# Performance work log

Hardware: AMD Instinct MI355X
Metric: run time of the kernel (lower is better)

## Reference

```python
import jax, jax.numpy as jnp
import numpy as np

A, B, M, H, MAX_NB, N_MOLS = 100000, 200000, 20000, 256, 10, 2000
ATOM_FDIM, BOND_FDIM, DEPTH = 35, 5, 3


def setup_inputs() -> dict:
    key = jax.random.key(0)
    ks = jax.random.split(key, 10)
    fatoms = jax.random.normal(ks[0], (A, ATOM_FDIM), dtype=jnp.float32)
    fbonds = jax.random.normal(ks[1], (B, ATOM_FDIM + BOND_FDIM), dtype=jnp.float32)
    agraph = jax.random.randint(ks[2], (A, MAX_NB), 0, M + B)
    bgraph = jax.random.randint(ks[3], (B, MAX_NB), 0, M + B)
    tree_message = jax.random.normal(ks[4], (M, H), dtype=jnp.float32)
    tree_message = tree_message.at[0].set(0.0)  # all_mess[0] is the zero pad vector
    atom_scope = jnp.sort(jax.random.randint(ks[5], (A,), 0, N_MOLS))
    s = 1.0 / np.sqrt(H)
    W_i = jax.random.normal(ks[6], (ATOM_FDIM + BOND_FDIM, H), dtype=jnp.float32) * s
    W_h = jax.random.normal(ks[7], (H, H), dtype=jnp.float32) * s
    W_o_w = jax.random.normal(ks[8], (ATOM_FDIM + H, H), dtype=jnp.float32) * s
    W_o_b = jax.random.normal(ks[9], (H,), dtype=jnp.float32) * s
    return {"fatoms": fatoms, "fbonds": fbonds, "agraph": agraph, "bgraph": bgraph,
            "tree_message": tree_message, "atom_scope": atom_scope,
            "W_i": W_i, "W_h": W_h, "W_o_w": W_o_w, "W_o_b": W_o_b}


def reference(fatoms, fbonds, agraph, bgraph, tree_message, atom_scope, W_i, W_h, W_o_w, W_o_b):
    binput = fbonds @ W_i                       # [B, H]
    graph_message = jax.nn.relu(binput)
    for _ in range(DEPTH - 1):
        message = jnp.concatenate([tree_message, graph_message], axis=0)  # [M+B, H]
        nei = message[bgraph].sum(axis=1)       # gather [B, MAX_NB, H] -> sum -> [B, H]
        graph_message = jax.nn.relu(binput + nei @ W_h)
    message = jnp.concatenate([tree_message, graph_message], axis=0)
    nei = message[agraph].sum(axis=1)           # [A, H]
    ainput = jnp.concatenate([fatoms, nei], axis=1)  # [A, ATOM_FDIM + H]
    atom_hiddens = jax.nn.relu(ainput @ W_o_w + W_o_b)
    # scope-based segment-mean pooling over atoms of each molecule
    sums = jax.ops.segment_sum(atom_hiddens, atom_scope, num_segments=N_MOLS)
    counts = jax.ops.segment_sum(jnp.ones((atom_hiddens.shape[0],), atom_hiddens.dtype),
                                 atom_scope, num_segments=N_MOLS)
    return sums / jnp.maximum(counts, 1.0)[:, None]
```

## Files before the change

kernel.cpp:

```cpp
#include <hip/hip_runtime.h>
#include <cstdint>
#include <cstddef>

#define A_N 100000
#define B_N 200000
#define M_N 20000
#define POOL_N 220000
#define HD 256
#define MAX_NB 10
#define N_MOLS 2000
#define ATOM_FDIM 35
#define FB_DIM 40

typedef unsigned short u16;
typedef __attribute__((ext_vector_type(8))) short bf16x8;
typedef __attribute__((ext_vector_type(4))) float f32x4;

__device__ u16 g_msg0[(size_t)B_N * HD];
__device__ u16 g_msg1[(size_t)B_N * HD];
__device__ u16 g_tmsgh[(size_t)M_N * HD];
__device__ u16 g_P[(size_t)POOL_N * HD];
__device__ u16 g_Q[(size_t)POOL_N * HD];
__device__ u16 g_binH[(size_t)B_N * HD];
__device__ u16 g_Fh[(size_t)A_N * HD];
__device__ u16 g_pWh_hi[65536], g_pWh_lo[65536];
__device__ u16 g_pWo_hi[65536], g_pWo_lo[65536];
__device__ int g_mstart[N_MOLS + 1];

__device__ __forceinline__ u16 f2b(float f)
{
    union { float f; unsigned u; } x; x.f = f;
    const unsigned r = x.u + 0x7FFFu + ((x.u >> 16) & 1u);
    return (u16)(r >> 16);
}
__device__ __forceinline__ float b2f(u16 h) { return __uint_as_float((unsigned)h << 16); }
__device__ __forceinline__ float blo(unsigned u) { return __uint_as_float(u << 16); }
__device__ __forceinline__ float bhi(unsigned u) { return __uint_as_float(u & 0xffff0000u); }

__device__ __forceinline__ int lbound(const int* __restrict__ s, int n, int v)
{
    int l = 0, r = n;
    while (l < r) { const int mid = (l + r) >> 1; if (s[mid] < v) l = mid + 1; else r = mid; }
    return l;
}

__device__ __forceinline__ void gl_lds16(const u16* g, u16* l)
{
    __builtin_amdgcn_global_load_lds(
        (const __attribute__((address_space(1))) unsigned int*)g,
        (__attribute__((address_space(3))) unsigned int*)l,
        16, 0, 0);
}

__global__ __launch_bounds__(256)
void k_setup(const float* __restrict__ tmsg,
             const float* __restrict__ Wh, const float* __restrict__ Wo,
             const int* __restrict__ scope)
{
    const int bid = blockIdx.x;
    const int tid = threadIdx.x;
    if (bid < 5000) {
        const int i = (bid * 256 + tid) * 4;
        if (i < M_N * HD) {
            const float4 v = *(const float4*)(tmsg + i);
            ushort4 o;
            o.x = f2b(v.x); o.y = f2b(v.y); o.z = f2b(v.z); o.w = f2b(v.w);
            *(ushort4*)(g_tmsgh + i) = o;
        }
    } else if (bid < 5032) {
        const int id = (bid - 5000) * 256 + tid;
        const int l = id & 63;
        const int t = (id >> 6) & 15;
        const int c = id >> 10;
        const int n = t * 16 + (l & 15);
        const int kb = c * 32 + ((l >> 4) << 3);
        const size_t base = (size_t)id * 8;
        #pragma unroll
        for (int j = 0; j < 8; ++j) {
            const int k = kb + j;
            const float wh = Wh[(size_t)k * HD + n];
            const u16 hh = f2b(wh);
            g_pWh_hi[base + j] = hh;
            g_pWh_lo[base + j] = f2b(wh - b2f(hh));
            const float wo = Wo[(size_t)(35 + k) * HD + n];
            const u16 oh = f2b(wo);
            g_pWo_hi[base + j] = oh;
            g_pWo_lo[base + j] = f2b(wo - b2f(oh));
        }
    } else {
        const int m = (bid - 5032) * 256 + tid;
        if (m <= N_MOLS) g_mstart[m] = lbound(scope, A_N, m);
    }
}

__global__ __launch_bounds__(256, 4)
void k_in(const float* __restrict__ fbonds, const float* __restrict__ Wi)
{
    const int lane = threadIdx.x & 63;
    const int wv   = threadIdx.x >> 6;
    const int c    = (wv & 1) * 128 + lane * 2;
    const int pair = (blockIdx.x * 4 + wv) >> 1;
    const int np   = gridDim.x * 2;

    float2 w[FB_DIM];
    #pragma unroll
    for (int k = 0; k < FB_DIM; ++k)
        w[k] = *(const float2*)&Wi[(size_t)k * HD + c];

    #pragma unroll 1
    for (int row = pair; row < B_N; row += np) {
        const float* fr = fbonds + (size_t)row * FB_DIM;
        float ax = 0.f, ay = 0.f;
        #pragma unroll
        for (int q = 0; q < FB_DIM / 4; ++q) {
            const float4 fv = *(const float4*)(fr + q * 4);
            ax += fv.x * w[q*4+0].x; ay += fv.x * w[q*4+0].y;
            ax += fv.y * w[q*4+1].x; ay += fv.y * w[q*4+1].y;
            ax += fv.z * w[q*4+2].x; ay += fv.z * w[q*4+2].y;
            ax += fv.w * w[q*4+3].x; ay += fv.w * w[q*4+3].y;
        }
        const size_t base = (size_t)row * HD + c;
        ushort2 bi; bi.x = f2b(ax); bi.y = f2b(ay);
        *(ushort2*)(g_binH + base) = bi;
        ushort2 o; o.x = f2b(fmaxf(ax, 0.f)); o.y = f2b(fmaxf(ay, 0.f));
        *(ushort2*)(g_msg0 + base) = o;
    }
}

__global__ __launch_bounds__(256, 2)
void k_gemmMF(int sel, int rowStart, int rowEnd)
{
    const u16* msrc = (sel == 1) ? g_msg1 : g_msg0;
    const u16* pHi  = (sel == 2) ? g_pWo_hi : g_pWh_hi;
    const u16* pLo  = (sel == 2) ? g_pWo_lo : g_pWh_lo;
    u16* dst        = (sel == 2) ? g_Q : g_P;

    __shared__ u16 lds[2][16384];

    const int tid  = threadIdx.x;
    const int lane = tid & 63;
    const int wv   = tid >> 6;
    const int l15  = lane & 15;
    const int quad = lane >> 4;
    const int tOff = (wv & 1) * 8;

    int rowIdeal[4];
    const u16* srow[4];
    #pragma unroll
    for (int rg = 0; rg < 4; ++rg) {
        const int ri = rowStart + blockIdx.x * 128 + (wv >> 1) * 64 + rg * 16 + l15;
        rowIdeal[rg] = ri;
        const int r = (ri < rowEnd) ? ri : (rowEnd - 1);
        srow[rg] = (r < M_N) ? (g_tmsgh + (size_t)r * HD)
                             : (msrc + (size_t)(r - M_N) * HD);
    }

    #define STAGE(bf, cc) do {                                            \
        const u16* sh_ = pHi + (cc) * 8192 + tid * 8;                     \
        const u16* sl_ = pLo + (cc) * 8192 + tid * 8;                     \
        u16* dh_ = &lds[bf][tid * 8];                                     \
        u16* dl_ = &lds[bf][8192 + tid * 8];                              \
        gl_lds16(sh_,        dh_);                                        \
        gl_lds16(sh_ + 2048, dh_ + 2048);                                 \
        gl_lds16(sh_ + 4096, dh_ + 4096);                                 \
        gl_lds16(sh_ + 6144, dh_ + 6144);                                 \
        gl_lds16(sl_,        dl_);                                        \
        gl_lds16(sl_ + 2048, dl_ + 2048);                                 \
        gl_lds16(sl_ + 4096, dl_ + 4096);                                 \
        gl_lds16(sl_ + 6144, dl_ + 6144);                                 \
    } while (0)

    f32x4 acc[4][8];
    #pragma unroll
    for (int rg = 0; rg < 4; ++rg)
        #pragma unroll
        for (int t = 0; t < 8; ++t)
            acc[rg][t] = (f32x4){0.f, 0.f, 0.f, 0.f};

    STAGE(0, 0);
    bf16x8 b0 = *(const bf16x8*)(srow[0] + quad * 8);
    bf16x8 b1 = *(const bf16x8*)(srow[1] + quad * 8);
    bf16x8 b2 = *(const bf16x8*)(srow[2] + quad * 8);
    bf16x8 b3 = *(const bf16x8*)(srow[3] + quad * 8);

    #pragma unroll 1
    for (int c = 0; c < 8; ++c) {
        __syncthreads();
        if (c < 7) STAGE((c + 1) & 1, c + 1);

        const int cn = (c + 1) & 7;
        const bf16x8 n0 = *(const bf16x8*)(srow[0] + cn * 32 + quad * 8);
        const bf16x8 n1 = *(const bf16x8*)(srow[1] + cn * 32 + quad * 8);
        const bf16x8 n2 = *(const bf16x8*)(srow[2] + cn * 32 + quad * 8);
        const bf16x8 n3 = *(const bf16x8*)(srow[3] + cn * 32 + quad * 8);

        const u16* Lh = &lds[c & 1][(size_t)tOff * 512 + lane * 8];
        const u16* Ll = Lh + 8192;
        #pragma unroll
        for (int t = 0; t < 8; ++t) {
            const bf16x8 ah = *(const bf16x8*)(Lh + t * 512);
            acc[0][t] = __builtin_amdgcn_mfma_f32_16x16x32_bf16(ah, b0, acc[0][t], 0, 0, 0);
            acc[1][t] = __builtin_amdgcn_mfma_f32_16x16x32_bf16(ah, b1, acc[1][t], 0, 0, 0);
            acc[2][t] = __builtin_amdgcn_mfma_f32_16x16x32_bf16(ah, b2, acc[2][t], 0, 0, 0);
            acc[3][t] = __builtin_amdgcn_mfma_f32_16x16x32_bf16(ah, b3, acc[3][t], 0, 0, 0);
            const bf16x8 al = *(const bf16x8*)(Ll + t * 512);
            acc[0][t] = __builtin_amdgcn_mfma_f32_16x16x32_bf16(al, b0, acc[0][t], 0, 0, 0);
            acc[1][t] = __builtin_amdgcn_mfma_f32_16x16x32_bf16(al, b1, acc[1][t], 0, 0, 0);
            acc[2][t] = __builtin_amdgcn_mfma_f32_16x16x32_bf16(al, b2, acc[2][t], 0, 0, 0);
            acc[3][t] = __builtin_amdgcn_mfma_f32_16x16x32_bf16(al, b3, acc[3][t], 0, 0, 0);
        }
        b0 = n0; b1 = n1; b2 = n2; b3 = n3;
    }
    #undef STAGE

    #pragma unroll
    for (int rg = 0; rg < 4; ++rg) {
        if (rowIdeal[rg] < rowEnd) {
            u16* drow = dst + (size_t)rowIdeal[rg] * HD + tOff * 16 + quad * 4;
            #pragma unroll
            for (int t = 0; t < 8; ++t) {
                ushort4 o;
                o.x = f2b(acc[rg][t][0]); o.y = f2b(acc[rg][t][1]);
                o.z = f2b(acc[rg][t][2]); o.w = f2b(acc[rg][t][3]);
                *(ushort4*)(drow + t * 16) = o;
            }
        }
    }
}

__global__ __launch_bounds__(256)
void k_gather(const int* __restrict__ bgraph, int dstSel, int rowOff)
{
    u16* dst = dstSel ? g_msg1 : g_msg0;
    __shared__ int idx_s[8][MAX_NB];
    const int tid = threadIdx.x;
    const int rowBase = rowOff + blockIdx.x * 8;
    if (tid < 8 * MAX_NB) {
        const int r = tid / MAX_NB;
        const int j = tid - r * MAX_NB;
        idx_s[r][j] = bgraph[(size_t)(rowBase + r) * MAX_NB + j];
    }
    __syncthreads();
    const int rl = tid >> 5;
    const int c  = (tid & 31) << 3;
    const int row = rowBase + rl;

    const uint4 bv = *(const uint4*)(g_binH + (size_t)row * HD + c);
    float s[8] = {0.f,0.f,0.f,0.f,0.f,0.f,0.f,0.f};
    #pragma unroll
    for (int j = 0; j < MAX_NB; ++j) {
        const uint4 v = *(const uint4*)(g_P + (size_t)idx_s[rl][j] * HD + c);
        s[0] += blo(v.x); s[1] += bhi(v.x);
        s[2] += blo(v.y); s[3] += bhi(v.y);
        s[4] += blo(v.z); s[5] += bhi(v.z);
        s[6] += blo(v.w); s[7] += bhi(v.w);
    }
    uint4 w;
    w.x = ((unsigned)f2b(fmaxf(s[0] + blo(bv.x), 0.f)))
        | ((unsigned)f2b(fmaxf(s[1] + bhi(bv.x), 0.f)) << 16);
    w.y = ((unsigned)f2b(fmaxf(s[2] + blo(bv.y), 0.f)))
        | ((unsigned)f2b(fmaxf(s[3] + bhi(bv.y), 0.f)) << 16);
    w.z = ((unsigned)f2b(fmaxf(s[4] + blo(bv.z), 0.f)))
        | ((unsigned)f2b(fmaxf(s[5] + bhi(bv.z), 0.f)) << 16);
    w.w = ((unsigned)f2b(fmaxf(s[6] + blo(bv.w), 0.f)))
        | ((unsigned)f2b(fmaxf(s[7] + bhi(bv.w), 0.f)) << 16);
    *(uint4*)(dst + (size_t)row * HD + c) = w;
}

__global__ __launch_bounds__(256, 4)
void k_F(const float* __restrict__ fatoms, const float* __restrict__ Wo,
         const float* __restrict__ bias)
{
    const int lane = threadIdx.x & 63;
    const int wv   = threadIdx.x >> 6;
    const int c    = (wv & 1) * 128 + lane * 2;
    const int pair = (blockIdx.x * 4 + wv) >> 1;
    const int np   = gridDim.x * 2;

    float2 w[ATOM_FDIM];
    #pragma unroll
    for (int k = 0; k < ATOM_FDIM; ++k)
        w[k] = *(const float2*)&Wo[(size_t)k * HD + c];
    const float2 b2 = *(const float2*)&bias[c];

    #pragma unroll 1
    for (int row = pair; row < A_N; row += np) {
        const float* fr = fatoms + (size_t)row * ATOM_FDIM;
        float ax = b2.x, ay = b2.y;
        #pragma unroll
        for (int q = 0; q < 8; ++q) {
            const float4 fv = *(const float4*)(fr + q * 4);
            ax += fv.x * w[q*4+0].x; ay += fv.x * w[q*4+0].y;
            ax += fv.y * w[q*4+1].x; ay += fv.y * w[q*4+1].y;
            ax += fv.z * w[q*4+2].x; ay += fv.z * w[q*4+2].y;
            ax += fv.w * w[q*4+3].x; ay += fv.w * w[q*4+3].y;
        }
        #pragma unroll
        for (int k = 32; k < ATOM_FDIM; ++k) {
            const float f = fr[k];
            ax += f * w[k].x; ay += f * w[k].y;
        }
        const size_t base = (size_t)row * HD + c;
        ushort2 o; o.x = f2b(ax); o.y = f2b(ay);
        *(ushort2*)(g_Fh + base) = o;
    }
}

__global__ __launch_bounds__(256)
void k_gatherA(const int* __restrict__ agraph, float* __restrict__ out)
{
    const int mol = blockIdx.x >> 1;
    const int ch  = (blockIdx.x & 1) * 128;
    const int tid = threadIdx.x;
    const int grp = tid >> 4;
    const int lc  = (tid & 15) * 8;
    const int c   = ch + lc;

    const int s0 = g_mstart[mol];
    const int s1 = g_mstart[mol + 1];

    float s[8] = {0.f,0.f,0.f,0.f,0.f,0.f,0.f,0.f};
    #pragma unroll 1
    for (int a = s0 + grp; a < s1; a += 16) {
        const int* ap = agraph + (size_t)a * MAX_NB;
        int idx[MAX_NB];
        #pragma unroll
        for (int j = 0; j < MAX_NB; ++j) idx[j] = ap[j];
        const uint4 fv = *(const uint4*)(g_Fh + (size_t)a * HD + c);
        float g0=0.f,g1=0.f,g2=0.f,g3=0.f,g4=0.f,g5=0.f,g6=0.f,g7=0.f;
        #pragma unroll
        for (int j = 0; j < MAX_NB; ++j) {
            const uint4 v = *(const uint4*)(g_Q + (size_t)idx[j] * HD + c);
            g0 += blo(v.x); g1 += bhi(v.x);
            g2 += blo(v.y); g3 += bhi(v.y);
            g4 += blo(v.z); g5 += bhi(v.z);
            g6 += blo(v.w); g7 += bhi(v.w);
        }
        s[0] += fmaxf(g0 + blo(fv.x), 0.f); s[1] += fmaxf(g1 + bhi(fv.x), 0.f);
        s[2] += fmaxf(g2 + blo(fv.y), 0.f); s[3] += fmaxf(g3 + bhi(fv.y), 0.f);
        s[4] += fmaxf(g4 + blo(fv.z), 0.f); s[5] += fmaxf(g5 + bhi(fv.z), 0.f);
        s[6] += fmaxf(g6 + blo(fv.w), 0.f); s[7] += fmaxf(g7 + bhi(fv.w), 0.f);
    }

    __shared__ float red[16][128];
    #pragma unroll
    for (int q = 0; q < 8; ++q) red[grp][lc + q] = s[q];
    __syncthreads();
    if (tid < 128) {
        float acc = 0.f;
        #pragma unroll
        for (int g = 0; g < 16; ++g) acc += red[g][tid];
        const float inv = 1.0f / fmaxf((float)(s1 - s0), 1.0f);
        out[(size_t)mol * HD + ch + tid] = acc * inv;
    }
}

extern "C" void kernel_launch(void* const* d_in, const int* in_sizes, int n_in,
                              void* d_out, int out_size, void* d_ws, size_t ws_size,
                              hipStream_t stream)
{
    const float* fatoms = (const float*)d_in[0];
    const float* fbonds = (const float*)d_in[1];
    const int*   agraph = (const int*)d_in[2];
    const int*   bgraph = (const int*)d_in[3];
    const float* tmsg   = (const float*)d_in[4];
    const int*   scope  = (const int*)d_in[5];
    const float* W_i    = (const float*)d_in[6];
    const float* W_h    = (const float*)d_in[7];
    const float* W_o    = (const float*)d_in[8];
    const float* W_ob   = (const float*)d_in[9];
    float* out = (float*)d_out;

    (void)d_ws; (void)ws_size;

    k_setup<<<5040, 256, 0, stream>>>(tmsg, W_h, W_o, scope);
    k_in<<<1024, 256, 0, stream>>>(fbonds, W_i);

    k_gemmMF<<<(POOL_N + 127) / 128, 256, 0, stream>>>(0, 0, POOL_N);
    for (int ch = 0; ch < 4; ++ch)
        k_gather<<<B_N / 32, 256, 0, stream>>>(bgraph, 1, ch * (B_N / 4));
    k_gemmMF<<<(B_N + 127) / 128, 256, 0, stream>>>(1, M_N, POOL_N);
    for (int ch = 0; ch < 4; ++ch)
        k_gather<<<B_N / 32, 256, 0, stream>>>(bgraph, 0, ch * (B_N / 4));

    k_gemmMF<<<(POOL_N + 127) / 128, 256, 0, stream>>>(2, 0, POOL_N);
    k_F<<<1024, 256, 0, stream>>>(fatoms, W_o, W_ob);
    k_gatherA<<<N_MOLS * 2, 256, 0, stream>>>(agraph, out);
}
```

Measured before the change: 1.209 ms.

## Stage feature rows in LDS for input projections and split gatherA over four chunks

k_in and k_F now copy 64-row tiles of fbonds/fatoms into shared memory with gl_lds16. Each thread then computes one output column across all tiled rows, instead of each wave re-reading rows from global memory with float2 weights. The aim is coalesced feature loads and less redundant global traffic, at the cost of narrower 2-byte stores and a serial 64-row inner loop. k_gatherA is split into four 64-column chunks per molecule with 32 row groups, which gives more blocks and more parallelism over atoms.

```diff
diff --git a/kernel.cpp b/kernel.cpp
--- a/kernel.cpp
+++ b/kernel.cpp
@@ -93,37 +93,42 @@
     }
 }
 
-__global__ __launch_bounds__(256, 4)
+__global__ __launch_bounds__(256)
 void k_in(const float* __restrict__ fbonds, const float* __restrict__ Wi)
 {
-    const int lane = threadIdx.x & 63;
-    const int wv   = threadIdx.x >> 6;
-    const int c    = (wv & 1) * 128 + lane * 2;
-    const int pair = (blockIdx.x * 4 + wv) >> 1;
-    const int np   = gridDim.x * 2;
-
-    float2 w[FB_DIM];
-    #pragma unroll
-    for (int k = 0; k < FB_DIM; ++k)
-        w[k] = *(const float2*)&Wi[(size_t)k * HD + c];
-
+    __shared__ float Lf[64 * FB_DIM];
+    const int tid = threadIdx.x;
+
+    float w[FB_DIM];
+    #pragma unroll
+    for (int k = 0; k < FB_DIM; ++k) w[k] = Wi[(size_t)k * HD + tid];
+
+    const int ntile = B_N / 64;
     #pragma unroll 1
-    for (int row = pair; row < B_N; row += np) {
-        const float* fr = fbonds + (size_t)row * FB_DIM;
-        float ax = 0.f, ay = 0.f;
-        #pragma unroll
-        for (int q = 0; q < FB_DIM / 4; ++q) {
-            const float4 fv = *(const float4*)(fr + q * 4);
-            ax += fv.x * w[q*4+0].x; ay += fv.x * w[q*4+0].y;
-            ax += fv.y * w[q*4+1].x; ay += fv.y * w[q*4+1].y;
-            ax += fv.z * w[q*4+2].x; ay += fv.z * w[q*4+2].y;
-            ax += fv.w * w[q*4+3].x; ay += fv.w * w[q*4+3].y;
-        }
-        const size_t base = (size_t)row * HD + c;
-        ushort2 bi; bi.x = f2b(ax); bi.y = f2b(ay);
-        *(ushort2*)(g_binH + base) = bi;
-        ushort2 o; o.x = f2b(fmaxf(ax, 0.f)); o.y = f2b(fmaxf(ay, 0.f));
-        *(ushort2*)(g_msg0 + base) = o;
+    for (int t = blockIdx.x; t < ntile; t += gridDim.x) {
+        const float* src = fbonds + (size_t)t * (64 * FB_DIM);
+        __syncthreads();
+        #pragma unroll
+        for (int i = 0; i < 3; ++i) {
+            const int g = i * 256 + tid;
+            if (g < 640) gl_lds16((const u16*)(src + g * 4), (u16*)(Lf + g * 4));
+        }
+        __syncthreads();
+        #pragma unroll 1
+        for (int r = 0; r < 64; ++r) {
+            const float* fr = Lf + r * FB_DIM;
+            float a0 = 0.f, a1 = 0.f;
+            #pragma unroll
+            for (int q = 0; q < FB_DIM / 4; ++q) {
+                const float4 fv = *(const float4*)(fr + q * 4);
+                a0 += fv.x * w[q*4+0] + fv.z * w[q*4+2];
+                a1 += fv.y * w[q*4+1] + fv.w * w[q*4+3];
+            }
+            const float acc = a0 + a1;
+            const size_t base = (size_t)(t * 64 + r) * HD + tid;
+            g_binH[base] = f2b(acc);
+            g_msg0[base] = f2b(fmaxf(acc, 0.f));
+        }
     }
 }
 
@@ -267,61 +272,64 @@
     *(uint4*)(dst + (size_t)row * HD + c) = w;
 }
 
-__global__ __launch_bounds__(256, 4)
+__global__ __launch_bounds__(256)
 void k_F(const float* __restrict__ fatoms, const float* __restrict__ Wo,
          const float* __restrict__ bias)
 {
-    const int lane = threadIdx.x & 63;
-    const int wv   = threadIdx.x >> 6;
-    const int c    = (wv & 1) * 128 + lane * 2;
-    const int pair = (blockIdx.x * 4 + wv) >> 1;
-    const int np   = gridDim.x * 2;
-
-    float2 w[ATOM_FDIM];
-    #pragma unroll
-    for (int k = 0; k < ATOM_FDIM; ++k)
-        w[k] = *(const float2*)&Wo[(size_t)k * HD + c];
-    const float2 b2 = *(const float2*)&bias[c];
-
+    __shared__ float Lf[64 * ATOM_FDIM];
+    const int tid = threadIdx.x;
+
+    float w[ATOM_FDIM];
+    #pragma unroll
+    for (int k = 0; k < ATOM_FDIM; ++k) w[k] = Wo[(size_t)k * HD + tid];
+    const float b = bias[tid];
+
+    const int ntile = (A_N + 63) / 64;
     #pragma unroll 1
-    for (int row = pair; row < A_N; row += np) {
-        const float* fr = fatoms + (size_t)row * ATOM_FDIM;
-        float ax = b2.x, ay = b2.y;
-        #pragma unroll
-        for (int q = 0; q < 8; ++q) {
-            const float4 fv = *(const float4*)(fr + q * 4);
-            ax += fv.x * w[q*4+0].x; ay += fv.x * w[q*4+0].y;
-            ax += fv.y * w[q*4+1].x; ay += fv.y * w[q*4+1].y;
-            ax += fv.z * w[q*4+2].x; ay += fv.z * w[q*4+2].y;
-            ax += fv.w * w[q*4+3].x; ay += fv.w * w[q*4+3].y;
-        }
-        #pragma unroll
-        for (int k = 32; k < ATOM_FDIM; ++k) {
-            const float f = fr[k];
-            ax += f * w[k].x; ay += f * w[k].y;
-        }
-        const size_t base = (size_t)row * HD + c;
-        ushort2 o; o.x = f2b(ax); o.y = f2b(ay);
-        *(ushort2*)(g_Fh + base) = o;
+    for (int t = blockIdx.x; t < ntile; t += gridDim.x) {
+        const int rows = (t * 64 + 64 <= A_N) ? 64 : (A_N - t * 64);
+        const int ng = rows * ATOM_FDIM / 4;
+        const float* src = fatoms + (size_t)t * (64 * ATOM_FDIM);
+        __syncthreads();
+        #pragma unroll
+        for (int i = 0; i < 3; ++i) {
+            const int g = i * 256 + tid;
+            if (g < ng) gl_lds16((const u16*)(src + g * 4), (u16*)(Lf + g * 4));
+        }
+        __syncthreads();
+        #pragma unroll 1
+        for (int r = 0; r < rows; ++r) {
+            const float* fr = Lf + r * ATOM_FDIM;
+            float a0 = b, a1 = 0.f;
+            #pragma unroll
+            for (int q = 0; q < 8; ++q) {
+                const float4 fv = *(const float4*)(fr + q * 4);
+                a0 += fv.x * w[q*4+0] + fv.z * w[q*4+2];
+                a1 += fv.y * w[q*4+1] + fv.w * w[q*4+3];
+            }
+            a0 += fr[32] * w[32] + fr[34] * w[34];
+            a1 += fr[33] * w[33];
+            g_Fh[(size_t)(t * 64 + r) * HD + tid] = f2b(a0 + a1);
+        }
     }
 }
 
 __global__ __launch_bounds__(256)
 void k_gatherA(const int* __restrict__ agraph, float* __restrict__ out)
 {
-    const int mol = blockIdx.x >> 1;
-    const int ch  = (blockIdx.x & 1) * 128;
-    const int tid = threadIdx.x;
-    const int grp = tid >> 4;
-    const int lc  = (tid & 15) * 8;
-    const int c   = ch + lc;
+    const int mol = blockIdx.x >> 2;
+    const int q   = blockIdx.x & 3;
+    const int tid = threadIdx.x;
+    const int grp = tid >> 3;
+    const int lc  = (tid & 7) * 8;
+    const int c   = q * 64 + lc;
 
     const int s0 = g_mstart[mol];
     const int s1 = g_mstart[mol + 1];
 
     float s[8] = {0.f,0.f,0.f,0.f,0.f,0.f,0.f,0.f};
     #pragma unroll 1
-    for (int a = s0 + grp; a < s1; a += 16) {
+    for (int a = s0 + grp; a < s1; a += 32) {
         const int* ap = agraph + (size_t)a * MAX_NB;
         int idx[MAX_NB];
         #pragma unroll
@@ -342,16 +350,16 @@
         s[6] += fmaxf(g6 + blo(fv.w), 0.f); s[7] += fmaxf(g7 + bhi(fv.w), 0.f);
     }
 
-    __shared__ float red[16][128];
-    #pragma unroll
-    for (int q = 0; q < 8; ++q) red[grp][lc + q] = s[q];
+    __shared__ float red[32][64];
+    #pragma unroll
+    for (int p = 0; p < 8; ++p) red[grp][lc + p] = s[p];
     __syncthreads();
-    if (tid < 128) {
+    if (tid < 64) {
         float acc = 0.f;
         #pragma unroll
-        for (int g = 0; g < 16; ++g) acc += red[g][tid];
+        for (int g = 0; g < 32; ++g) acc += red[g][tid];
         const float inv = 1.0f / fmaxf((float)(s1 - s0), 1.0f);
-        out[(size_t)mol * HD + ch + tid] = acc * inv;
+        out[(size_t)mol * HD + q * 64 + tid] = acc * inv;
     }
 }
 
@@ -374,7 +382,7 @@
     (void)d_ws; (void)ws_size;
 
     k_setup<<<5040, 256, 0, stream>>>(tmsg, W_h, W_o, scope);
-    k_in<<<1024, 256, 0, stream>>>(fbonds, W_i);
+    k_in<<<2048, 256, 0, stream>>>(fbonds, W_i);
 
     k_gemmMF<<<(POOL_N + 127) / 128, 256, 0, stream>>>(0, 0, POOL_N);
     for (int ch = 0; ch < 4; ++ch)
@@ -384,6 +392,6 @@
         k_gather<<<B_N / 32, 256, 0, stream>>>(bgraph, 0, ch * (B_N / 4));
 
     k_gemmMF<<<(POOL_N + 127) / 128, 256, 0, stream>>>(2, 0, POOL_N);
-    k_F<<<1024, 256, 0, stream>>>(fatoms, W_o, W_ob);
-    k_gatherA<<<N_MOLS * 2, 256, 0, stream>>>(agraph, out);
-}
+    k_F<<<1563, 256, 0, stream>>>(fatoms, W_o, W_ob);
+    k_gatherA<<<N_MOLS * 4, 256, 0, stream>>>(agraph, out);
+}
```

Measured after the change: 1.406 ms. 1.16x slower.
